# Kernel tuning notes

Measured on AMD Instinct MI355X. Metric: run time of the kernel, lower is better.

The kernel has to match this reference:

```python
import jax, jax.numpy as jnp
import numpy as np

N = 8192      # number of tree nodes
H = 256       # lstm_hiddens
D = 300       # word_dims (in_dim)
V = 50000     # vocab (n_embed)
K = 4         # max children per node (4-ary tree)
OUT = 4       # category_num


def _make_tree():
    # Static 4-ary tree: node i's children are 4i+1..4i+4 (if < N).
    idx = np.arange(N)[:, None] * K + 1 + np.arange(K)[None, :]
    mask = (idx < N).astype(np.float32)
    idx = np.where(idx < N, idx, 0)
    return jnp.asarray(idx, dtype=jnp.int32), jnp.asarray(mask, dtype=jnp.float32)


def setup_inputs() -> dict:
    key = jax.random.key(0)
    ks = jax.random.split(key, 6)
    xs = jax.random.randint(ks[0], (N,), 0, V, dtype=jnp.int32)
    emb_table = jax.random.normal(ks[1], (V, D), jnp.float32) * 0.1
    Wx = jax.random.normal(ks[2], (4, H, D), jnp.float32) * (1.0 / np.sqrt(D))
    bx = jnp.zeros((4, H), jnp.float32)
    Wh = jax.random.normal(ks[3], (4, H, H), jnp.float32) * (1.0 / np.sqrt(H))
    bh = jnp.zeros((4, H), jnp.float32)
    Wout = jax.random.normal(ks[4], (OUT, H), jnp.float32) * (1.0 / np.sqrt(H))
    bout = jnp.zeros((OUT,), jnp.float32)
    child_idx, child_mask = _make_tree()
    return dict(xs=xs, child_idx=child_idx, child_mask=child_mask,
                emb_table=emb_table, Wx=Wx, bx=bx, Wh=Wh, bh=bh,
                Wout=Wout, bout=bout)


def reference(xs, child_idx, child_mask, emb_table, Wx, bx, Wh, bh, Wout, bout):
    # Embedding lookup (dropout is identity in eval)
    X = emb_table[xs]                                   # [N, D]
    # Precompute all x-side gate projections in one batched matmul.
    # Gate order: 0=i, 1=f, 2=o, 3=u  (matches ix/fx/ox/ux).
    gx = jnp.einsum('ghd,nd->ngh', Wx, X) + bx          # [N, 4, H]

    Wh_i, Wh_f, Wh_o, Wh_u = Wh[0], Wh[1], Wh[2], Wh[3]
    bh_i, bh_f, bh_o, bh_u = bh[0], bh[1], bh[2], bh[3]

    def step(carry, i):
        Hbuf, Cbuf = carry
        cidx = child_idx[i]                              # [K]
        m = child_mask[i][:, None]                       # [K, 1]
        Hc = Hbuf[cidx] * m                              # [K, H] masked child h
        Cc = Cbuf[cidx] * m                              # [K, H] masked child c
        hs = Hc.sum(0)                                   # child_h_sum
        g = gx[i]                                        # [4, H]
        ig = jax.nn.sigmoid(g[0] + Wh_i @ hs + bh_i)
        og = jax.nn.sigmoid(g[2] + Wh_o @ hs + bh_o)
        ug = jnp.tanh(g[3] + Wh_u @ hs + bh_u)
        f = jax.nn.sigmoid(g[1] + Hc @ Wh_f.T + bh_f)    # [K, H] per-child forget
        c = ig * ug + (f * Cc).sum(0)                    # masked children have Cc=0
        h = og * jnp.tanh(c)
        return (Hbuf.at[i].set(h), Cbuf.at[i].set(c)), None

    order = jnp.arange(N - 1, -1, -1)                    # children before parents
    init = (jnp.zeros((N, H), X.dtype), jnp.zeros((N, H), X.dtype))
    (Hbuf, _), _ = jax.lax.scan(step, init, order)

    logits = Wout @ Hbuf[0] + bout                       # root output
    return jax.nn.log_softmax(logits)
```

## Files before the change

kernel.cpp:

```cpp
#include <hip/hip_runtime.h>


#define N_NODES 8192
#define HDIM 256
#define DDIM 300
#define GXC 1024
#define LEAF_FIRST 2048
#define WH_STRIDE 65536
#define XI(k) ((k) + (((k) >> 6) << 2))

__device__ __forceinline__ float sigf(float x) { return 1.0f / (1.0f + __expf(-x)); }

__global__ __launch_bounds__(256) void gx_gemm(
    const int* __restrict__ xs, const float* __restrict__ emb,
    const float* __restrict__ Wx, const float* __restrict__ bx,
    float* __restrict__ gx)
{
    const int lid  = blockIdx.x + blockIdx.y * gridDim.x;
    const int rowt = (lid & 7) * 8 + ((lid >> 3) & 7);
    const int colt = lid >> 6;
    const int n0 = rowt * 128;
    const int c0 = colt * 64;
    if (n0 >= LEAF_FIRST && colt >= 4 && colt < 8) return;

    __shared__ __align__(16) float As[16][132];
    __shared__ __align__(16) float Bs[16][68];
    const int tid   = threadIdx.x;
    const int sr    = tid >> 1;
    const int sk8   = (tid & 1) << 3;
    const int sbr   = tid >> 2;
    const int sbk   = (tid & 3) << 2;
    const int trow4 = (tid >> 4) << 2;
    const int tcol4 = (tid & 15) << 2;

    const long arow = (long)xs[n0 + sr] * DDIM;
    const long brow = (long)(c0 + sbr) * DDIM;

    float acc[8][4] = {};

    float4 a0 = *(const float4*)(emb + arow + sk8);
    float4 a1 = *(const float4*)(emb + arow + sk8 + 4);
    float4 b0 = *(const float4*)(Wx  + brow + sbk);

    for (int k0 = 0; k0 < DDIM; k0 += 16) {
        __syncthreads();
        As[sk8+0][sr] = a0.x; As[sk8+1][sr] = a0.y; As[sk8+2][sr] = a0.z; As[sk8+3][sr] = a0.w;
        As[sk8+4][sr] = a1.x; As[sk8+5][sr] = a1.y; As[sk8+6][sr] = a1.z; As[sk8+7][sr] = a1.w;
        Bs[sbk+0][sbr] = b0.x; Bs[sbk+1][sbr] = b0.y; Bs[sbk+2][sbr] = b0.z; Bs[sbk+3][sbr] = b0.w;
        __syncthreads();

        const int kn = k0 + 16;
        a0 = make_float4(0.f,0.f,0.f,0.f); a1 = a0; b0 = a0;
        if (kn < DDIM) {
            if (kn + sk8 < DDIM) a0 = *(const float4*)(emb + arow + kn + sk8);
            if (kn + sk8 + 4 < DDIM) a1 = *(const float4*)(emb + arow + kn + sk8 + 4);
            if (kn + sbk < DDIM) b0 = *(const float4*)(Wx + brow + kn + sbk);
        }

        #pragma unroll
        for (int k = 0; k < 16; k++) {
            const float4 av0 = *(const float4*)&As[k][trow4];
            const float4 av1 = *(const float4*)&As[k][64 + trow4];
            const float4 bv  = *(const float4*)&Bs[k][tcol4];
            const float aa[8] = {av0.x,av0.y,av0.z,av0.w,av1.x,av1.y,av1.z,av1.w};
            const float bb[4] = {bv.x,bv.y,bv.z,bv.w};
            #pragma unroll
            for (int i = 0; i < 8; i++)
                #pragma unroll
                for (int j = 0; j < 4; j++)
                    acc[i][j] = fmaf(aa[i], bb[j], acc[i][j]);
        }
    }

    const float4 bxa = *(const float4*)(bx + c0 + tcol4);
    #pragma unroll
    for (int i = 0; i < 8; i++) {
        const int row = n0 + ((i < 4) ? (trow4 + i) : (64 + trow4 + i - 4));
        float4 r0;
        r0.x = acc[i][0] + bxa.x; r0.y = acc[i][1] + bxa.y;
        r0.z = acc[i][2] + bxa.z; r0.w = acc[i][3] + bxa.w;
        *(float4*)(gx + (long)row * GXC + c0 + tcol4) = r0;
    }
}

__global__ __launch_bounds__(256) void leaf_kernel(
    const float* __restrict__ gx, const float* __restrict__ bh,
    float* __restrict__ Hb, float* __restrict__ Cb)
{
    const int t = threadIdx.x;
    const float bi = bh[t], bo = bh[512 + t], bu = bh[768 + t];
    #pragma unroll
    for (int s = 0; s < 4; s++) {
        const int node = LEAF_FIRST + blockIdx.x * 4 + s;
        const float* g = gx + (long)node * GXC;
        const float gi = g[t]       + bi;
        const float go = g[512 + t] + bo;
        const float gu = g[768 + t] + bu;
        const float c  = sigf(gi) * tanhf(gu);
        const float h  = sigf(go) * tanhf(c);
        Hb[(long)node * HDIM + t] = h;
        Cb[(long)node * HDIM + t] = c;
    }
}

__global__ __launch_bounds__(256) void level_gemm(
    int first, int M, const float* __restrict__ Hb,
    const int* __restrict__ child_idx, const float* __restrict__ child_mask,
    const float* __restrict__ Wh, float* __restrict__ D)
{
    __shared__ __align__(16) float Xs[16][68];
    __shared__ __align__(16) float Ws[16][68];
    const int tid  = threadIdx.x;
    const int sec  = blockIdx.y;
    const int c0   = blockIdx.x * 64;
    const int r0   = blockIdx.z * 64;
    const int sr   = tid >> 2;
    const int sk   = (tid & 3) << 2;
    const int trow = (tid >> 4) << 2;
    const int tcol = (tid & 15) << 2;

    const float* Wg;
    if      (sec == 0) Wg = Wh;
    else if (sec == 1) Wg = Wh + 2 * WH_STRIDE;
    else if (sec == 2) Wg = Wh + 3 * WH_STRIDE;
    else               Wg = Wh + 1 * WH_STRIDE;

    const int  nl    = c0 + sr;
    const bool valid = nl < M;
    int   ci[4];
    float cm[4] = {0.f, 0.f, 0.f, 0.f};
    if (valid) {
        const int n = first + nl;
        if (sec < 3) {
            #pragma unroll
            for (int k = 0; k < 4; k++) {
                ci[k] = child_idx[n * 4 + k];
                cm[k] = child_mask[n * 4 + k];
            }
        } else {
            ci[0] = child_idx[n * 4 + (sec - 3)];
            cm[0] = child_mask[n * 4 + (sec - 3)];
        }
    }
    const long wrow = (long)(r0 + sr) * HDIM;

    float acc[4][4] = {};
    float4 hvr[4], wvr;

    #pragma unroll
    for (int k = 0; k < 4; k++) hvr[k] = make_float4(0.f, 0.f, 0.f, 0.f);
    if (valid) {
        if (sec < 3) {
            #pragma unroll
            for (int k = 0; k < 4; k++)
                if (cm[k] != 0.f)
                    hvr[k] = *(const float4*)(Hb + ci[k] * HDIM + sk);
        } else if (cm[0] != 0.f) {
            hvr[0] = *(const float4*)(Hb + ci[0] * HDIM + sk);
        }
    }
    wvr = *(const float4*)(Wg + wrow + sk);

    for (int k0 = 0; k0 < HDIM; k0 += 16) {
        __syncthreads();
        float4 xv;
        xv.x = hvr[0].x + hvr[1].x + hvr[2].x + hvr[3].x;
        xv.y = hvr[0].y + hvr[1].y + hvr[2].y + hvr[3].y;
        xv.z = hvr[0].z + hvr[1].z + hvr[2].z + hvr[3].z;
        xv.w = hvr[0].w + hvr[1].w + hvr[2].w + hvr[3].w;
        Xs[sk+0][sr] = xv.x; Xs[sk+1][sr] = xv.y; Xs[sk+2][sr] = xv.z; Xs[sk+3][sr] = xv.w;
        Ws[sk+0][sr] = wvr.x; Ws[sk+1][sr] = wvr.y; Ws[sk+2][sr] = wvr.z; Ws[sk+3][sr] = wvr.w;
        __syncthreads();

        const int kn = k0 + 16;
        if (kn < HDIM) {
            #pragma unroll
            for (int k = 0; k < 4; k++) hvr[k] = make_float4(0.f, 0.f, 0.f, 0.f);
            if (valid) {
                if (sec < 3) {
                    #pragma unroll
                    for (int k = 0; k < 4; k++)
                        if (cm[k] != 0.f)
                            hvr[k] = *(const float4*)(Hb + ci[k] * HDIM + kn + sk);
                } else if (cm[0] != 0.f) {
                    hvr[0] = *(const float4*)(Hb + ci[0] * HDIM + kn + sk);
                }
            }
            wvr = *(const float4*)(Wg + wrow + kn + sk);
        }

        #pragma unroll
        for (int k = 0; k < 16; k++) {
            float4 a = *(const float4*)&Ws[k][trow];
            float4 b = *(const float4*)&Xs[k][tcol];
            float avv[4] = {a.x, a.y, a.z, a.w};
            float bvv[4] = {b.x, b.y, b.z, b.w};
            #pragma unroll
            for (int i = 0; i < 4; i++)
                #pragma unroll
                for (int j = 0; j < 4; j++)
                    acc[i][j] = fmaf(avv[i], bvv[j], acc[i][j]);
        }
    }

    #pragma unroll
    for (int j = 0; j < 4; j++) {
        const int col = c0 + tcol + j;
        if (col < M) {
            float4 r;
            r.x = acc[0][j]; r.y = acc[1][j]; r.z = acc[2][j]; r.w = acc[3][j];
            *(float4*)(D + ((long)(sec * M + col)) * HDIM + r0 + trow) = r;
        }
    }
}

__global__ __launch_bounds__(256) void level_pointwise(
    int first, int M, int do_out,
    const float* __restrict__ gx, const float* __restrict__ D,
    const int* __restrict__ child_idx, const float* __restrict__ child_mask,
    const float* __restrict__ bh, float* __restrict__ Hb, float* __restrict__ Cb,
    const float* __restrict__ Wout, const float* __restrict__ bout,
    float* __restrict__ out)
{
    __shared__ float hroot[HDIM];
    __shared__ float logits[4];
    const int nl = blockIdx.x;
    const int n  = first + nl;
    const int t  = threadIdx.x;
    const float di  = D[((long)(0 * M + nl)) * HDIM + t];
    const float dO  = D[((long)(1 * M + nl)) * HDIM + t];
    const float du  = D[((long)(2 * M + nl)) * HDIM + t];
    const float* g = gx + (long)n * GXC;
    const float gi  = g[t]       + bh[t]       + di;
    const float gfb = g[256 + t] + bh[256 + t];
    const float go  = g[512 + t] + bh[512 + t] + dO;
    const float gu  = g[768 + t] + bh[768 + t] + du;

    float c = sigf(gi) * tanhf(gu);
    #pragma unroll
    for (int k = 0; k < 4; k++) {
        const float m = child_mask[n * 4 + k];
        if (m != 0.f) {
            const float df = D[((long)((3 + k) * M + nl)) * HDIM + t];
            const float cc = Cb[(long)child_idx[n * 4 + k] * HDIM + t];
            c = fmaf(sigf(gfb + df), cc, c);
        }
    }
    const float h = sigf(go) * tanhf(c);
    Hb[(long)n * HDIM + t] = h;
    Cb[(long)n * HDIM + t] = c;

    if (do_out) {
        hroot[t] = h;
        __syncthreads();
        const int o    = t >> 6;
        const int lane = t & 63;
        float s = 0.f;
        for (int jj = lane; jj < HDIM; jj += 64)
            s = fmaf(Wout[o * HDIM + jj], hroot[jj], s);
        #pragma unroll
        for (int off = 32; off > 0; off >>= 1)
            s += __shfl_down(s, off, 64);
        if (lane == 0) logits[o] = s + bout[o];
        __syncthreads();
        if (t == 0) {
            float m = logits[0];
            #pragma unroll
            for (int i = 1; i < 4; i++) m = fmaxf(m, logits[i]);
            float se = 0.f;
            #pragma unroll
            for (int i = 0; i < 4; i++) se += __expf(logits[i] - m);
            const float lse = m + __logf(se);
            #pragma unroll
            for (int i = 0; i < 4; i++) out[i] = logits[i] - lse;
        }
    }
}

__global__ __launch_bounds__(256) void tail_fused(
    int first, int M,
    const float* __restrict__ gx, const int* __restrict__ child_idx,
    const float* __restrict__ child_mask, const float* __restrict__ Wh,
    const float* __restrict__ bh, float* __restrict__ Hb, float* __restrict__ Cb)
{
    __shared__ __align__(16) float Xc[4][272];
    __shared__ __align__(16) float Xh[272];
    __shared__ float Ds[7][64];

    const int t  = threadIdx.x;
    const int nl = blockIdx.x;
    const int rb = blockIdx.y;
    const int n  = first + nl;

    {
        const int ch = t >> 6;
        const int e4 = (t & 63) << 2;
        const int cidx = child_idx[n * 4 + ch];
        const float m  = child_mask[n * 4 + ch];
        float4 v = make_float4(0.f, 0.f, 0.f, 0.f);
        if (m != 0.f) v = *(const float4*)(Hb + (long)cidx * HDIM + e4);
        *(float4*)&Xc[ch][XI(e4)] = v;
    }
    __syncthreads();
    {
        const int k = t;
        Xh[XI(k)] = Xc[0][XI(k)] + Xc[1][XI(k)] + Xc[2][XI(k)] + Xc[3][XI(k)];
    }
    __syncthreads();

    const int q = t >> 2, j = t & 3;
    const int row = rb * 64 + q;
    const float* Wi = Wh + 0 * WH_STRIDE + (long)row * HDIM;
    const float* Wf = Wh + 1 * WH_STRIDE + (long)row * HDIM;
    const float* Wo = Wh + 2 * WH_STRIDE + (long)row * HDIM;
    const float* Wu = Wh + 3 * WH_STRIDE + (long)row * HDIM;

    float a[7] = {};
    #pragma unroll 4
    for (int kk = j * 64; kk < j * 64 + 64; kk += 4) {
        const float4 wi = *(const float4*)(Wi + kk);
        const float4 wo = *(const float4*)(Wo + kk);
        const float4 wu = *(const float4*)(Wu + kk);
        const float4 wf = *(const float4*)(Wf + kk);
        const float4 hs = *(const float4*)&Xh[XI(kk)];
        a[0] += wi.x*hs.x + wi.y*hs.y + wi.z*hs.z + wi.w*hs.w;
        a[1] += wo.x*hs.x + wo.y*hs.y + wo.z*hs.z + wo.w*hs.w;
        a[2] += wu.x*hs.x + wu.y*hs.y + wu.z*hs.z + wu.w*hs.w;
        #pragma unroll
        for (int ch = 0; ch < 4; ch++) {
            const float4 cv = *(const float4*)&Xc[ch][XI(kk)];
            a[3 + ch] += wf.x*cv.x + wf.y*cv.y + wf.z*cv.z + wf.w*cv.w;
        }
    }
    #pragma unroll
    for (int s = 0; s < 7; s++) {
        float v = a[s];
        v += __shfl_xor(v, 1, 64);
        v += __shfl_xor(v, 2, 64);
        if (j == 0) Ds[s][q] = v;
    }
    __syncthreads();

    if (t < 64) {
        const int r = rb * 64 + t;
        const float* g = gx + (long)n * GXC;
        const float gi  = g[r]       + bh[r]       + Ds[0][t];
        const float gfb = g[256 + r] + bh[256 + r];
        const float go  = g[512 + r] + bh[512 + r] + Ds[1][t];
        const float gu  = g[768 + r] + bh[768 + r] + Ds[2][t];
        float c = sigf(gi) * tanhf(gu);
        #pragma unroll
        for (int ch = 0; ch < 4; ch++) {
            const float m = child_mask[n * 4 + ch];
            if (m != 0.f) {
                const float cc = Cb[(long)child_idx[n * 4 + ch] * HDIM + r];
                c = fmaf(sigf(gfb + Ds[3 + ch][t]), cc, c);
            }
        }
        const float h = sigf(go) * tanhf(c);
        Hb[(long)n * HDIM + r] = h;
        Cb[(long)n * HDIM + r] = c;
    }
}

extern "C" void kernel_launch(void* const* d_in, const int* in_sizes, int n_in,
                              void* d_out, int out_size, void* d_ws, size_t ws_size,
                              hipStream_t stream)
{
    const int*   xs         = (const int*)  d_in[0];
    const int*   child_idx  = (const int*)  d_in[1];
    const float* child_mask = (const float*)d_in[2];
    const float* emb        = (const float*)d_in[3];
    const float* Wx         = (const float*)d_in[4];
    const float* bx         = (const float*)d_in[5];
    const float* Wh         = (const float*)d_in[6];
    const float* bh         = (const float*)d_in[7];
    const float* Wout       = (const float*)d_in[8];
    const float* bout       = (const float*)d_in[9];
    float* out = (float*)d_out;

    float* gxb = (float*)d_ws;
    float* Hb  = gxb + (size_t)N_NODES * GXC;
    float* Cb  = Hb  + (size_t)N_NODES * HDIM;
    float* Dbuf = gxb + (size_t)LEAF_FIRST * GXC;

    gx_gemm<<<dim3(16, 64), 256, 0, stream>>>(xs, emb, Wx, bx, gxb);
    leaf_kernel<<<(N_NODES - LEAF_FIRST) / 4, 256, 0, stream>>>(gxb, bh, Hb, Cb);

    const int pfb[3] = {1365, 341, 85};
    const int pcb[3] = { 683, 1024, 256};
    for (int p = 0; p < 3; p++) {
        const int M = pcb[p];
        dim3 grid((M + 63) / 64, 7, 4);
        level_gemm<<<grid, 256, 0, stream>>>(pfb[p], M, Hb, child_idx, child_mask,
                                             Wh, Dbuf);
        level_pointwise<<<M, 256, 0, stream>>>(pfb[p], M, 0, gxb, Dbuf, child_idx,
                                               child_mask, bh, Hb, Cb,
                                               Wout, bout, out);
    }

    const int pft[3] = {21, 5, 1};
    const int pct[3] = {64, 16, 4};
    for (int p = 0; p < 3; p++) {
        dim3 grid(pct[p], 4);
        tail_fused<<<grid, 256, 0, stream>>>(pft[p], pct[p], gxb, child_idx,
                                             child_mask, Wh, bh, Hb, Cb);
    }

    {
        dim3 grid(1, 7, 4);
        level_gemm<<<grid, 256, 0, stream>>>(0, 1, Hb, child_idx, child_mask,
                                             Wh, Dbuf);
        level_pointwise<<<1, 256, 0, stream>>>(0, 1, 1, gxb, Dbuf, child_idx,
                                               child_mask, bh, Hb, Cb,
                                               Wout, bout, out);
    }
}
```

Measured before the change: 306.2 us.

## Fuse leaf LSTM pointwise into the gx GEMM epilogue for leaf nodes

Merges the x-projection GEMM and the leaf kernel into one launch. Blocks 0-511 compute all four gate projections for internal nodes (rows below 2048) with 64x64 tiles. Blocks 512-895 compute only the i/o/u gates for leaf nodes and apply the sigmoid/tanh epilogue in registers, writing H and C directly. This avoids writing leaf gx to global memory and reading it back, and removes one launch. In exchange the tiles are smaller (64 rows instead of 128), there are more blocks, and the leaf blocks carry three accumulator sets, which raises register pressure.

```diff
diff --git a/kernel.cpp b/kernel.cpp
--- a/kernel.cpp
+++ b/kernel.cpp
@@ -11,95 +11,152 @@
 
 __device__ __forceinline__ float sigf(float x) { return 1.0f / (1.0f + __expf(-x)); }
 
-__global__ __launch_bounds__(256) void gx_gemm(
+__global__ __launch_bounds__(256) void gx_leaf_gemm(
     const int* __restrict__ xs, const float* __restrict__ emb,
     const float* __restrict__ Wx, const float* __restrict__ bx,
-    float* __restrict__ gx)
-{
-    const int lid  = blockIdx.x + blockIdx.y * gridDim.x;
-    const int rowt = (lid & 7) * 8 + ((lid >> 3) & 7);
-    const int colt = lid >> 6;
-    const int n0 = rowt * 128;
-    const int c0 = colt * 64;
-    if (n0 >= LEAF_FIRST && colt >= 4 && colt < 8) return;
-
-    __shared__ __align__(16) float As[16][132];
-    __shared__ __align__(16) float Bs[16][68];
-    const int tid   = threadIdx.x;
-    const int sr    = tid >> 1;
-    const int sk8   = (tid & 1) << 3;
-    const int sbr   = tid >> 2;
-    const int sbk   = (tid & 3) << 2;
-    const int trow4 = (tid >> 4) << 2;
-    const int tcol4 = (tid & 15) << 2;
-
-    const long arow = (long)xs[n0 + sr] * DDIM;
-    const long brow = (long)(c0 + sbr) * DDIM;
-
-    float acc[8][4] = {};
-
-    float4 a0 = *(const float4*)(emb + arow + sk8);
-    float4 a1 = *(const float4*)(emb + arow + sk8 + 4);
-    float4 b0 = *(const float4*)(Wx  + brow + sbk);
-
-    for (int k0 = 0; k0 < DDIM; k0 += 16) {
-        __syncthreads();
-        As[sk8+0][sr] = a0.x; As[sk8+1][sr] = a0.y; As[sk8+2][sr] = a0.z; As[sk8+3][sr] = a0.w;
-        As[sk8+4][sr] = a1.x; As[sk8+5][sr] = a1.y; As[sk8+6][sr] = a1.z; As[sk8+7][sr] = a1.w;
-        Bs[sbk+0][sbr] = b0.x; Bs[sbk+1][sbr] = b0.y; Bs[sbk+2][sbr] = b0.z; Bs[sbk+3][sbr] = b0.w;
-        __syncthreads();
-
-        const int kn = k0 + 16;
-        a0 = make_float4(0.f,0.f,0.f,0.f); a1 = a0; b0 = a0;
-        if (kn < DDIM) {
-            if (kn + sk8 < DDIM) a0 = *(const float4*)(emb + arow + kn + sk8);
-            if (kn + sk8 + 4 < DDIM) a1 = *(const float4*)(emb + arow + kn + sk8 + 4);
-            if (kn + sbk < DDIM) b0 = *(const float4*)(Wx + brow + kn + sbk);
-        }
-
-        #pragma unroll
-        for (int k = 0; k < 16; k++) {
-            const float4 av0 = *(const float4*)&As[k][trow4];
-            const float4 av1 = *(const float4*)&As[k][64 + trow4];
-            const float4 bv  = *(const float4*)&Bs[k][tcol4];
-            const float aa[8] = {av0.x,av0.y,av0.z,av0.w,av1.x,av1.y,av1.z,av1.w};
-            const float bb[4] = {bv.x,bv.y,bv.z,bv.w};
-            #pragma unroll
-            for (int i = 0; i < 8; i++)
-                #pragma unroll
-                for (int j = 0; j < 4; j++)
-                    acc[i][j] = fmaf(aa[i], bb[j], acc[i][j]);
-        }
-    }
-
-    const float4 bxa = *(const float4*)(bx + c0 + tcol4);
-    #pragma unroll
-    for (int i = 0; i < 8; i++) {
-        const int row = n0 + ((i < 4) ? (trow4 + i) : (64 + trow4 + i - 4));
-        float4 r0;
-        r0.x = acc[i][0] + bxa.x; r0.y = acc[i][1] + bxa.y;
-        r0.z = acc[i][2] + bxa.z; r0.w = acc[i][3] + bxa.w;
-        *(float4*)(gx + (long)row * GXC + c0 + tcol4) = r0;
-    }
-}
-
-__global__ __launch_bounds__(256) void leaf_kernel(
-    const float* __restrict__ gx, const float* __restrict__ bh,
+    const float* __restrict__ bh, float* __restrict__ gx,
     float* __restrict__ Hb, float* __restrict__ Cb)
 {
-    const int t = threadIdx.x;
-    const float bi = bh[t], bo = bh[512 + t], bu = bh[768 + t];
-    #pragma unroll
-    for (int s = 0; s < 4; s++) {
-        const int node = LEAF_FIRST + blockIdx.x * 4 + s;
-        const float* g = gx + (long)node * GXC;
-        const float gi = g[t]       + bi;
-        const float go = g[512 + t] + bo;
-        const float gu = g[768 + t] + bu;
-        const float c  = sigf(gi) * tanhf(gu);
-        const float h  = sigf(go) * tanhf(c);
-        Hb[(long)node * HDIM + t] = h;
-        Cb[(long)node * HDIM + t] = c;
+    __shared__ __align__(16) float As[16][68];
+    __shared__ __align__(16) float Bs[3][16][68];
+    const int lid  = blockIdx.x;
+    const int tid  = threadIdx.x;
+    const int sr   = tid >> 2;
+    const int sk   = (tid & 3) << 2;
+    const int trow = (tid >> 4) << 2;
+    const int tcol = (tid & 15) << 2;
+
+    if (lid < 512) {
+        const int xcd = lid & 7, idx = lid >> 3;
+        const int n0 = (xcd * 4 + (idx & 3)) * 64;
+        const int c0 = (idx >> 2) * 64;
+
+        const long arow = (long)xs[n0 + sr] * DDIM;
+        const long brow = (long)(c0 + sr) * DDIM;
+
+        float acc[4][4] = {};
+        float4 av = *(const float4*)(emb + arow + sk);
+        float4 bv = *(const float4*)(Wx  + brow + sk);
+
+        for (int k0 = 0; k0 < DDIM; k0 += 16) {
+            __syncthreads();
+            As[sk+0][sr] = av.x; As[sk+1][sr] = av.y; As[sk+2][sr] = av.z; As[sk+3][sr] = av.w;
+            Bs[0][sk+0][sr] = bv.x; Bs[0][sk+1][sr] = bv.y; Bs[0][sk+2][sr] = bv.z; Bs[0][sk+3][sr] = bv.w;
+            __syncthreads();
+
+            const int kn = k0 + 16;
+            av = make_float4(0.f,0.f,0.f,0.f); bv = av;
+            if (kn + sk < DDIM) {
+                av = *(const float4*)(emb + arow + kn + sk);
+                bv = *(const float4*)(Wx  + brow + kn + sk);
+            }
+
+            #pragma unroll
+            for (int k = 0; k < 16; k++) {
+                float4 a = *(const float4*)&As[k][trow];
+                float4 b = *(const float4*)&Bs[0][k][tcol];
+                float aa[4] = {a.x, a.y, a.z, a.w};
+                float bb[4] = {b.x, b.y, b.z, b.w};
+                #pragma unroll
+                for (int i = 0; i < 4; i++)
+                    #pragma unroll
+                    for (int j = 0; j < 4; j++)
+                        acc[i][j] = fmaf(aa[i], bb[j], acc[i][j]);
+            }
+        }
+
+        const int col = c0 + tcol;
+        const float4 bxa = *(const float4*)(bx + col);
+        #pragma unroll
+        for (int i = 0; i < 4; i++) {
+            float4 r;
+            r.x = acc[i][0] + bxa.x; r.y = acc[i][1] + bxa.y;
+            r.z = acc[i][2] + bxa.z; r.w = acc[i][3] + bxa.w;
+            *(float4*)(gx + (long)(n0 + trow + i) * GXC + col) = r;
+        }
+    } else {
+        const int l   = lid - 512;
+        const int xcd = l & 7, idx = l >> 3;
+        const int n0  = LEAF_FIRST + (xcd * 12 + idx % 12) * 64;
+        const int c0  = (idx / 12) * 64;
+
+        const long arow = (long)xs[n0 + sr] * DDIM;
+        const long brow0 = (long)(c0 + sr) * DDIM;
+        const long brow1 = (long)(512 + c0 + sr) * DDIM;
+        const long brow2 = (long)(768 + c0 + sr) * DDIM;
+
+        float acc[3][4][4] = {};
+        float4 av = *(const float4*)(emb + arow + sk);
+        float4 b0 = *(const float4*)(Wx + brow0 + sk);
+        float4 b1 = *(const float4*)(Wx + brow1 + sk);
+        float4 b2 = *(const float4*)(Wx + brow2 + sk);
+
+        for (int k0 = 0; k0 < DDIM; k0 += 16) {
+            __syncthreads();
+            As[sk+0][sr] = av.x; As[sk+1][sr] = av.y; As[sk+2][sr] = av.z; As[sk+3][sr] = av.w;
+            Bs[0][sk+0][sr] = b0.x; Bs[0][sk+1][sr] = b0.y; Bs[0][sk+2][sr] = b0.z; Bs[0][sk+3][sr] = b0.w;
+            Bs[1][sk+0][sr] = b1.x; Bs[1][sk+1][sr] = b1.y; Bs[1][sk+2][sr] = b1.z; Bs[1][sk+3][sr] = b1.w;
+            Bs[2][sk+0][sr] = b2.x; Bs[2][sk+1][sr] = b2.y; Bs[2][sk+2][sr] = b2.z; Bs[2][sk+3][sr] = b2.w;
+            __syncthreads();
+
+            const int kn = k0 + 16;
+            av = make_float4(0.f,0.f,0.f,0.f); b0 = av; b1 = av; b2 = av;
+            if (kn + sk < DDIM) {
+                av = *(const float4*)(emb + arow + kn + sk);
+                b0 = *(const float4*)(Wx + brow0 + kn + sk);
+                b1 = *(const float4*)(Wx + brow1 + kn + sk);
+                b2 = *(const float4*)(Wx + brow2 + kn + sk);
+            }
+
+            #pragma unroll
+            for (int k = 0; k < 16; k++) {
+                float4 a = *(const float4*)&As[k][trow];
+                float aa[4] = {a.x, a.y, a.z, a.w};
+                #pragma unroll
+                for (int g = 0; g < 3; g++) {
+                    float4 b = *(const float4*)&Bs[g][k][tcol];
+                    float bb[4] = {b.x, b.y, b.z, b.w};
+                    #pragma unroll
+                    for (int i = 0; i < 4; i++)
+                        #pragma unroll
+                        for (int j = 0; j < 4; j++)
+                            acc[g][i][j] = fmaf(aa[i], bb[j], acc[g][i][j]);
+                }
+            }
+        }
+
+        const int colg = c0 + tcol;
+        const float4 bxi = *(const float4*)(bx + colg);
+        const float4 bxo = *(const float4*)(bx + 512 + colg);
+        const float4 bxu = *(const float4*)(bx + 768 + colg);
+        const float4 bhi = *(const float4*)(bh + colg);
+        const float4 bho = *(const float4*)(bh + 512 + colg);
+        const float4 bhu = *(const float4*)(bh + 768 + colg);
+        const float bxiv[4] = {bxi.x,bxi.y,bxi.z,bxi.w};
+        const float bxov[4] = {bxo.x,bxo.y,bxo.z,bxo.w};
+        const float bxuv[4] = {bxu.x,bxu.y,bxu.z,bxu.w};
+        const float bhiv[4] = {bhi.x,bhi.y,bhi.z,bhi.w};
+        const float bhov[4] = {bho.x,bho.y,bho.z,bho.w};
+        const float bhuv[4] = {bhu.x,bhu.y,bhu.z,bhu.w};
+        #pragma unroll
+        for (int i = 0; i < 4; i++) {
+            const long row = (long)(n0 + trow + i) * HDIM + colg;
+            float4 hv, cv;
+            float hh[4], cc[4];
+            #pragma unroll
+            for (int j = 0; j < 4; j++) {
+                const float gi = (acc[0][i][j] + bxiv[j]) + bhiv[j];
+                const float go = (acc[1][i][j] + bxov[j]) + bhov[j];
+                const float gu = (acc[2][i][j] + bxuv[j]) + bhuv[j];
+                const float c  = sigf(gi) * tanhf(gu);
+                const float h  = sigf(go) * tanhf(c);
+                cc[j] = c; hh[j] = h;
+            }
+            hv.x = hh[0]; hv.y = hh[1]; hv.z = hh[2]; hv.w = hh[3];
+            cv.x = cc[0]; cv.y = cc[1]; cv.z = cc[2]; cv.w = cc[3];
+            *(float4*)(Hb + row) = hv;
+            *(float4*)(Cb + row) = cv;
+        }
     }
 }
 
@@ -384,8 +441,7 @@
     float* Cb  = Hb  + (size_t)N_NODES * HDIM;
     float* Dbuf = gxb + (size_t)LEAF_FIRST * GXC;
 
-    gx_gemm<<<dim3(16, 64), 256, 0, stream>>>(xs, emb, Wx, bx, gxb);
-    leaf_kernel<<<(N_NODES - LEAF_FIRST) / 4, 256, 0, stream>>>(gxb, bh, Hb, Cb);
+    gx_leaf_gemm<<<896, 256, 0, stream>>>(xs, emb, Wx, bx, bh, gxb, Hb, Cb);
 
     const int pfb[3] = {1365, 341, 85};
     const int pcb[3] = { 683, 1024, 256};
```

Result: faster. 299.8 us (-2.1%).
